# Kernel tuning notes

Hardware: AMD Instinct MI355X
Metric: run time of the kernel (lower is better)

## Reference

```python
import jax, jax.numpy as jnp
import numpy as np

N = 50000      # nodes
E = 800000     # edges (before self-loops)
H = 4          # attention heads
C = 32         # out_features per head
DIN = 128      # in_features (== H*C so residual path is active)
ED = 16        # edge_dim
NEG = 0.2      # LeakyReLU negative slope (GATConv default)
EPS = 1e-5     # LayerNorm eps


def setup_inputs() -> dict:
    key = jax.random.key(0)
    ks = jax.random.split(key, 12)
    s = 0.05
    return {
        "x": jax.random.normal(ks[0], (N, DIN), dtype=jnp.float32),
        "edge_index": jax.random.randint(ks[1], (2, E), 0, N, dtype=jnp.int64),
        "edge_attr": jax.random.normal(ks[2], (E, ED), dtype=jnp.float32),
        # edge_processor: Linear(ED, ED) + ReLU (dropout = identity at eval)
        "W_ep": jax.random.normal(ks[3], (ED, ED), dtype=jnp.float32) * s,
        "b_ep": jnp.zeros((ED,), dtype=jnp.float32),
        # GATConv params (lin / lin_edge are bias-free in PyG)
        "W_lin": jax.random.normal(ks[4], (DIN, H * C), dtype=jnp.float32) * s,
        "W_edge": jax.random.normal(ks[5], (ED, H * C), dtype=jnp.float32) * s,
        "att_src": jax.random.normal(ks[6], (H, C), dtype=jnp.float32) * s,
        "att_dst": jax.random.normal(ks[7], (H, C), dtype=jnp.float32) * s,
        "att_edge": jax.random.normal(ks[8], (H, C), dtype=jnp.float32) * s,
        "bias": jnp.zeros((H * C,), dtype=jnp.float32),
        # LayerNorm params
        "ln_g": jnp.ones((H * C,), dtype=jnp.float32),
        "ln_b": jnp.zeros((H * C,), dtype=jnp.float32),
    }


def reference(x, edge_index, edge_attr, W_ep, b_ep, W_lin, W_edge,
              att_src, att_dst, att_edge, bias, ln_g, ln_b):
    n = x.shape[0]
    src, dst = edge_index[0], edge_index[1]

    # edge_processor: Linear + ReLU
    ea = jax.nn.relu(edge_attr @ W_ep + b_ep)                       # [E, ED]

    # add self-loops (PyG GATConv default), loop edge_attr = mean of incoming
    ones = jnp.ones((ea.shape[0],), dtype=ea.dtype)
    deg = jax.ops.segment_sum(ones, dst, num_segments=n)            # [N]
    loop_attr = jax.ops.segment_sum(ea, dst, num_segments=n)
    loop_attr = loop_attr / jnp.maximum(deg, 1.0)[:, None]          # [N, ED]
    loop = jnp.arange(n, dtype=src.dtype)
    src2 = jnp.concatenate([src, loop])                             # [E+N]
    dst2 = jnp.concatenate([dst, loop])
    ea2 = jnp.concatenate([ea, loop_attr], axis=0)                  # [E+N, ED]

    # node / edge linear transforms
    h = (x @ W_lin).reshape(n, H, C)                                # [N, H, C]
    a_src = jnp.einsum('nhc,hc->nh', h, att_src)                    # [N, H]
    a_dst = jnp.einsum('nhc,hc->nh', h, att_dst)
    e = (ea2 @ W_edge).reshape(-1, H, C)                            # [E+N, H, C]
    a_e = jnp.einsum('ehc,hc->eh', e, att_edge)                     # [E+N, H]

    # per-edge attention logits + leaky relu
    alpha = a_src[src2] + a_dst[dst2] + a_e                         # [E+N, H]
    alpha = jnp.where(alpha >= 0, alpha, NEG * alpha)

    # segment softmax over incoming edges of each dst node
    m = jax.ops.segment_max(alpha, dst2, num_segments=n)            # [N, H]
    ex = jnp.exp(alpha - m[dst2])
    denom = jax.ops.segment_sum(ex, dst2, num_segments=n)           # [N, H]
    w = ex / denom[dst2]                                            # [E+N, H]

    # scatter-aggregate messages
    msg = h[src2] * w[:, :, None]                                   # [E+N, H, C]
    out = jax.ops.segment_sum(msg, dst2, num_segments=n)            # [N, H, C]
    out = out.reshape(n, H * C) + bias

    # residual (DIN == H*C) + LayerNorm
    out = out + x
    mu = jnp.mean(out, axis=-1, keepdims=True)
    var = jnp.var(out, axis=-1, keepdims=True)
    out = (out - mu) * jax.lax.rsqrt(var + EPS) * ln_g + ln_b
    return out
```

## Files before the change

kernel.cpp:

```cpp
#include <hip/hip_runtime.h>
#include <hip/hip_fp16.h>
#include <math.h>

#define NN   50000
#define EE   800000
#define HH   4
#define CC   32
#define DINN 128
#define ED   16
#define NEGS 0.2f
#define LNEPS 1e-5f
#define CPAD 32
#define SLOT 64

struct __align__(16) Hp4 { __half2 a, b, c, d; };

__global__ __launch_bounds__(256, 3) void k_node(
        const float* __restrict__ x, const float* __restrict__ W_lin,
        const float* __restrict__ att_src, const float* __restrict__ att_dst,
        __half* __restrict__ hb, float* __restrict__ a_src, float* __restrict__ a_dst,
        int* __restrict__ cnt) {
    __shared__ float xr[64 * 132];
    int t = threadIdx.x;
    int row0 = blockIdx.x * 64;

    #pragma unroll
    for (int i = 0; i < 8; ++i) {
        int idx = blockIdx.x * 2048 + i * 256 + t;
        if (idx < NN * CPAD) cnt[idx] = 0;
    }

    #pragma unroll
    for (int i = 0; i < 8; ++i) {
        int idx = t + 256 * i;
        int r = idx >> 5, kq = idx & 31;
        int row = row0 + r;
        float4 v = make_float4(0.f, 0.f, 0.f, 0.f);
        if (row < NN) v = ((const float4*)x)[(long)row * 32 + kq];
        *(float4*)&xr[r * 132 + kq * 4] = v;
    }
    __syncthreads();

    int colg = t & 15, rowg = t >> 4;
    int c0 = colg * 8;
    const float* Wp = W_lin + c0;
    float acc[4][8] = {};

    #pragma unroll 2
    for (int k = 0; k < DINN; k += 2) {
        float4 wa0 = *(const float4*)&Wp[(long)k * DINN];
        float4 wb0 = *(const float4*)&Wp[(long)k * DINN + 4];
        float4 wa1 = *(const float4*)&Wp[(long)(k + 1) * DINN];
        float4 wb1 = *(const float4*)&Wp[(long)(k + 1) * DINN + 4];
        #pragma unroll
        for (int i = 0; i < 4; ++i) {
            float2 xv = *(const float2*)&xr[(rowg * 4 + i) * 132 + k];
            acc[i][0] = fmaf(xv.x, wa0.x, acc[i][0]);
            acc[i][1] = fmaf(xv.x, wa0.y, acc[i][1]);
            acc[i][2] = fmaf(xv.x, wa0.z, acc[i][2]);
            acc[i][3] = fmaf(xv.x, wa0.w, acc[i][3]);
            acc[i][4] = fmaf(xv.x, wb0.x, acc[i][4]);
            acc[i][5] = fmaf(xv.x, wb0.y, acc[i][5]);
            acc[i][6] = fmaf(xv.x, wb0.z, acc[i][6]);
            acc[i][7] = fmaf(xv.x, wb0.w, acc[i][7]);
            acc[i][0] = fmaf(xv.y, wa1.x, acc[i][0]);
            acc[i][1] = fmaf(xv.y, wa1.y, acc[i][1]);
            acc[i][2] = fmaf(xv.y, wa1.z, acc[i][2]);
            acc[i][3] = fmaf(xv.y, wa1.w, acc[i][3]);
            acc[i][4] = fmaf(xv.y, wb1.x, acc[i][4]);
            acc[i][5] = fmaf(xv.y, wb1.y, acc[i][5]);
            acc[i][6] = fmaf(xv.y, wb1.z, acc[i][6]);
            acc[i][7] = fmaf(xv.y, wb1.w, acc[i][7]);
        }
    }

    int head = colg >> 2;
    int cw = c0 & 31;
    float4 as0 = *(const float4*)&att_src[head * CC + cw];
    float4 as1 = *(const float4*)&att_src[head * CC + cw + 4];
    float4 ad0 = *(const float4*)&att_dst[head * CC + cw];
    float4 ad1 = *(const float4*)&att_dst[head * CC + cw + 4];
    #pragma unroll
    for (int i = 0; i < 4; ++i) {
        int row = row0 + rowg * 4 + i;
        if (row < NN) {
            Hp4 p;
            p.a = __floats2half2_rn(acc[i][0], acc[i][1]);
            p.b = __floats2half2_rn(acc[i][2], acc[i][3]);
            p.c = __floats2half2_rn(acc[i][4], acc[i][5]);
            p.d = __floats2half2_rn(acc[i][6], acc[i][7]);
            *(Hp4*)&hb[(long)row * DINN + c0] = p;
        }
        float ps = acc[i][0]*as0.x + acc[i][1]*as0.y + acc[i][2]*as0.z + acc[i][3]*as0.w
                 + acc[i][4]*as1.x + acc[i][5]*as1.y + acc[i][6]*as1.z + acc[i][7]*as1.w;
        float pd = acc[i][0]*ad0.x + acc[i][1]*ad0.y + acc[i][2]*ad0.z + acc[i][3]*ad0.w
                 + acc[i][4]*ad1.x + acc[i][5]*ad1.y + acc[i][6]*ad1.z + acc[i][7]*ad1.w;
        ps += __shfl_xor(ps, 1); ps += __shfl_xor(ps, 2);
        pd += __shfl_xor(pd, 1); pd += __shfl_xor(pd, 2);
        if ((colg & 3) == 0 && row < NN) {
            a_src[row * 4 + head] = ps;
            a_dst[row * 4 + head] = pd;
        }
    }
}

__device__ __forceinline__ void edge_compute(
        float4 A0, float4 A1, float4 A2, float4 A3,
        const float* __restrict__ Wl, const float* __restrict__ bl,
        const float* __restrict__ vl,
        int src, int dst, int rk, uint4* __restrict__ pk) {
    float a[ED];
    a[0]=A0.x; a[1]=A0.y; a[2]=A0.z; a[3]=A0.w;
    a[4]=A1.x; a[5]=A1.y; a[6]=A1.z; a[7]=A1.w;
    a[8]=A2.x; a[9]=A2.y; a[10]=A2.z; a[11]=A2.w;
    a[12]=A3.x; a[13]=A3.y; a[14]=A3.z; a[15]=A3.w;

    float r[ED];
    #pragma unroll
    for (int j = 0; j < ED; ++j) r[j] = bl[j];
    #pragma unroll
    for (int d = 0; d < ED; ++d) {
        float av = a[d];
        #pragma unroll
        for (int j = 0; j < ED; ++j) r[j] = fmaf(av, Wl[d * ED + j], r[j]);
    }

    float ae0 = 0.f, ae1 = 0.f, ae2 = 0.f, ae3 = 0.f;
    #pragma unroll
    for (int d = 0; d < ED; ++d) {
        float rd = fmaxf(r[d], 0.f);
        ae0 = fmaf(rd, vl[d * 4 + 0], ae0);
        ae1 = fmaf(rd, vl[d * 4 + 1], ae1);
        ae2 = fmaf(rd, vl[d * 4 + 2], ae2);
        ae3 = fmaf(rd, vl[d * 4 + 3], ae3);
    }

    __half2 ae01 = __floats2half2_rn(ae0, ae1);
    __half2 ae23 = __floats2half2_rn(ae2, ae3);
    if (rk < SLOT) {
        long q = (long)dst * SLOT + rk;
        pk[q] = make_uint4(*(unsigned*)&ae01, *(unsigned*)&ae23,
                           (unsigned)src, 0u);
    }
}

__global__ __launch_bounds__(256) void k_edgeA(
        const int* __restrict__ ei, const float* __restrict__ edge_attr,
        const float* __restrict__ W_ep, const float* __restrict__ b_ep,
        const float* __restrict__ W_edge, const float* __restrict__ att_edge,
        int* __restrict__ cnt, uint4* __restrict__ pk) {
    __shared__ float Wl[ED * ED];
    __shared__ float bl[ED];
    __shared__ float vl[ED * 4];
    int t = threadIdx.x;
    if (t < ED * ED) Wl[t] = W_ep[t];
    if (t < ED) bl[t] = b_ep[t];
    if (t >= 192 && t < 192 + 64) {
        int q = t - 192;
        int d = q >> 2, h = q & 3;
        float s = 0.f;
        #pragma unroll 8
        for (int c = 0; c < CC; ++c)
            s += W_edge[d * (HH * CC) + h * CC + c] * att_edge[h * CC + c];
        vl[q] = s;
    }
    __syncthreads();

    int e0 = blockIdx.x * 512 + t;
    int e1 = e0 + 256;

    if ((blockIdx.x + 1) * 512 <= EE) {
        int s0 = ei[e0], s1 = ei[e1];
        int d0 = ei[EE + e0], d1 = ei[EE + e1];

        const float4* ap0 = (const float4*)(edge_attr + (long)e0 * ED);
        const float4* ap1 = (const float4*)(edge_attr + (long)e1 * ED);
        float4 A0 = ap0[0], A1 = ap0[1], A2 = ap0[2], A3 = ap0[3];
        float4 B0 = ap1[0], B1 = ap1[1], B2 = ap1[2], B3 = ap1[3];

        int rk0 = atomicAdd(cnt + (long)d0 * CPAD, 1);
        int rk1 = atomicAdd(cnt + (long)d1 * CPAD, 1);

        edge_compute(A0, A1, A2, A3, Wl, bl, vl, s0, d0, rk0, pk);
        edge_compute(B0, B1, B2, B3, Wl, bl, vl, s1, d1, rk1, pk);
    } else {
        #pragma unroll
        for (int u = 0; u < 2; ++u) {
            int e = e0 + u * 256;
            if (e >= EE) break;
            int src = ei[e];
            int dst = ei[EE + e];
            const float4* ap = (const float4*)(edge_attr + (long)e * ED);
            float4 A0 = ap[0], A1 = ap[1], A2 = ap[2], A3 = ap[3];
            int rk = atomicAdd(cnt + (long)dst * CPAD, 1);
            edge_compute(A0, A1, A2, A3, Wl, bl, vl, src, dst, rk, pk);
        }
    }
}

#define AGG_STEP(qq, hh, AA)                                      \
    do {                                                          \
        unsigned aw_ = (head & 2) ? (qq).y : (qq).x;              \
        float2 aef_ = __half22float2(*(__half2*)&aw_);            \
        float ae_ = (head & 1) ? aef_.y : aef_.x;                 \
        float v_ = (AA) + adn + ae_;                              \
        v_ = (v_ >= 0.f) ? v_ : NEGS * v_;                        \
        float w_ = __expf(v_);                                    \
        s_own += w_;                                              \
        aes_own += ae_;                                           \
        float2 hf_ = __half22float2(hh);                          \
        accx = fmaf(w_, hf_.x, accx);                             \
        accy = fmaf(w_, hf_.y, accy);                             \
    } while (0)

__global__ __launch_bounds__(256) void k_aggregate(
        const float* __restrict__ x, const __half2* __restrict__ hb,
        const float* __restrict__ a_src, const float* __restrict__ a_dst,
        const int* __restrict__ cnt, const uint4* __restrict__ pk,
        const float* __restrict__ bias, const float* __restrict__ ln_g,
        const float* __restrict__ ln_b, float* __restrict__ out) {
    int t = threadIdx.x;
    int wave = t >> 6, lane = t & 63;
    int n = blockIdx.x * 4 + wave;
    if (n >= NN) return;

    int deg = cnt[(long)n * CPAD];
    if (deg > SLOT) deg = SLOT;
    const uint4* rp = pk + (long)n * SLOT;
    int head = lane >> 4;

    float adn = a_dst[n * 4 + head];
    float accx = 0.f, accy = 0.f, s_own = 0.f, aes_own = 0.f;

    int k = 0;
    for (; k + 8 <= deg; k += 8) {
        uint4 q0 = rp[k + 0], q1 = rp[k + 1], q2 = rp[k + 2], q3 = rp[k + 3];
        uint4 q4 = rp[k + 4], q5 = rp[k + 5], q6 = rp[k + 6], q7 = rp[k + 7];
        int s0 = (int)q0.z, s1 = (int)q1.z, s2 = (int)q2.z, s3 = (int)q3.z;
        int s4 = (int)q4.z, s5 = (int)q5.z, s6 = (int)q6.z, s7 = (int)q7.z;
        __half2 h0 = hb[(long)s0 * 64 + lane], h1 = hb[(long)s1 * 64 + lane];
        __half2 h2 = hb[(long)s2 * 64 + lane], h3 = hb[(long)s3 * 64 + lane];
        __half2 h4 = hb[(long)s4 * 64 + lane], h5 = hb[(long)s5 * 64 + lane];
        __half2 h6 = hb[(long)s6 * 64 + lane], h7 = hb[(long)s7 * 64 + lane];
        float A0 = a_src[s0 * 4 + head], A1 = a_src[s1 * 4 + head];
        float A2 = a_src[s2 * 4 + head], A3 = a_src[s3 * 4 + head];
        float A4 = a_src[s4 * 4 + head], A5 = a_src[s5 * 4 + head];
        float A6 = a_src[s6 * 4 + head], A7 = a_src[s7 * 4 + head];
        AGG_STEP(q0, h0, A0); AGG_STEP(q1, h1, A1);
        AGG_STEP(q2, h2, A2); AGG_STEP(q3, h3, A3);
        AGG_STEP(q4, h4, A4); AGG_STEP(q5, h5, A5);
        AGG_STEP(q6, h6, A6); AGG_STEP(q7, h7, A7);
    }
    for (; k < deg; ++k) {
        uint4 q0 = rp[k];
        int s0 = (int)q0.z;
        __half2 h0 = hb[(long)s0 * 64 + lane];
        float A0 = a_src[s0 * 4 + head];
        AGG_STEP(q0, h0, A0);
    }

    float asn = a_src[n * 4 + head];
    float inv_deg = 1.0f / fmaxf((float)deg, 1.0f);
    float v = asn + adn + aes_own * inv_deg;
    v = (v >= 0.f) ? v : NEGS * v;
    float w0 = __expf(v);
    s_own += w0;
    float2 hn = __half22float2(hb[(long)n * 64 + lane]);
    accx = fmaf(w0, hn.x, accx);
    accy = fmaf(w0, hn.y, accy);
    float is = 1.0f / s_own;
    accx *= is; accy *= is;

    int c0 = lane * 2;
    float2 b2 = *(const float2*)&bias[c0];
    float2 x2 = *(const float2*)&x[(long)n * DINN + c0];
    float oa = accx + b2.x + x2.x;
    float ob = accy + b2.y + x2.y;
    float sum = oa + ob, sumsq = oa * oa + ob * ob;
    #pragma unroll
    for (int d2 = 1; d2 < 64; d2 <<= 1) {
        sum   += __shfl_xor(sum, d2);
        sumsq += __shfl_xor(sumsq, d2);
    }
    float mu  = sum * (1.0f / DINN);
    float var = sumsq * (1.0f / DINN) - mu * mu;
    float rs  = rsqrtf(var + LNEPS);
    float2 g2  = *(const float2*)&ln_g[c0];
    float2 lb2 = *(const float2*)&ln_b[c0];
    float2 o2;
    o2.x = (oa - mu) * rs * g2.x + lb2.x;
    o2.y = (ob - mu) * rs * g2.y + lb2.y;
    *(float2*)&out[(long)n * DINN + c0] = o2;
}

extern "C" void kernel_launch(void* const* d_in, const int* in_sizes, int n_in,
                              void* d_out, int out_size, void* d_ws, size_t ws_size,
                              hipStream_t stream) {
    const float* x         = (const float*)d_in[0];
    const int*   ei        = (const int*)d_in[1];
    const float* edge_attr = (const float*)d_in[2];
    const float* W_ep      = (const float*)d_in[3];
    const float* b_ep      = (const float*)d_in[4];
    const float* W_lin     = (const float*)d_in[5];
    const float* W_edge    = (const float*)d_in[6];
    const float* att_src   = (const float*)d_in[7];
    const float* att_dst   = (const float*)d_in[8];
    const float* att_edge  = (const float*)d_in[9];
    const float* bias      = (const float*)d_in[10];
    const float* ln_g      = (const float*)d_in[11];
    const float* ln_b      = (const float*)d_in[12];
    float* out = (float*)d_out;

    char* ws = (char*)d_ws;
    size_t o = 0;
    auto take = [&](size_t bytes) -> char* {
        char* p = ws + o;
        o = (o + bytes + 255) & ~(size_t)255;
        return p;
    };
    __half* hbuf  = (__half*)take((size_t)NN * DINN * 2);
    float*  a_src = (float*)take((size_t)NN * 4 * 4);
    float*  a_dst = (float*)take((size_t)NN * 4 * 4);
    int*    cnt   = (int*)  take((size_t)NN * CPAD * 4);
    uint4*  pk    = (uint4*)take((size_t)NN * SLOT * 16);

    k_node<<<(NN + 63) / 64, 256, 0, stream>>>(x, W_lin, att_src, att_dst,
                                               hbuf, a_src, a_dst, cnt);
    k_edgeA<<<(EE + 511) / 512, 256, 0, stream>>>(ei, edge_attr, W_ep, b_ep,
                                                  W_edge, att_edge, cnt, pk);
    k_aggregate<<<(NN + 3) / 4, 256, 0, stream>>>(x, (const __half2*)hbuf,
                                                  a_src, a_dst, cnt,
                                                  (const uint4*)pk,
                                                  bias, ln_g, ln_b, out);
}
```

Measured before the change: 268.9 us.

## Fuse node projection and edge kernels into one interleaved launch

Merges the node linear-projection kernel and the edge-processing kernel into a single launch. Every third block does node GEMM work and the rest do edge work, so the compute-heavy node blocks and the atomic/memory-heavy edge blocks can run concurrently and one kernel boundary disappears. Because edge blocks now increment counters while node blocks may still be running, counter zeroing moves to a separate hipMemsetAsync. In exchange, edge blocks now reserve the node path's large shared-memory buffer and share its launch bounds, which may lower their occupancy.

New measurement: 267.5 us. About the same (-0.5%).

```diff
diff --git a/kernel.cpp b/kernel.cpp
--- a/kernel.cpp
+++ b/kernel.cpp
@@ -13,96 +13,11 @@
 #define CPAD 32
 #define SLOT 64
 
+#define NBLK_NODE 782
+#define NBLK_EDGE 1563
+#define NBLK_FUSED (NBLK_NODE + NBLK_EDGE)
+
 struct __align__(16) Hp4 { __half2 a, b, c, d; };
-
-__global__ __launch_bounds__(256, 3) void k_node(
-        const float* __restrict__ x, const float* __restrict__ W_lin,
-        const float* __restrict__ att_src, const float* __restrict__ att_dst,
-        __half* __restrict__ hb, float* __restrict__ a_src, float* __restrict__ a_dst,
-        int* __restrict__ cnt) {
-    __shared__ float xr[64 * 132];
-    int t = threadIdx.x;
-    int row0 = blockIdx.x * 64;
-
-    #pragma unroll
-    for (int i = 0; i < 8; ++i) {
-        int idx = blockIdx.x * 2048 + i * 256 + t;
-        if (idx < NN * CPAD) cnt[idx] = 0;
-    }
-
-    #pragma unroll
-    for (int i = 0; i < 8; ++i) {
-        int idx = t + 256 * i;
-        int r = idx >> 5, kq = idx & 31;
-        int row = row0 + r;
-        float4 v = make_float4(0.f, 0.f, 0.f, 0.f);
-        if (row < NN) v = ((const float4*)x)[(long)row * 32 + kq];
-        *(float4*)&xr[r * 132 + kq * 4] = v;
-    }
-    __syncthreads();
-
-    int colg = t & 15, rowg = t >> 4;
-    int c0 = colg * 8;
-    const float* Wp = W_lin + c0;
-    float acc[4][8] = {};
-
-    #pragma unroll 2
-    for (int k = 0; k < DINN; k += 2) {
-        float4 wa0 = *(const float4*)&Wp[(long)k * DINN];
-        float4 wb0 = *(const float4*)&Wp[(long)k * DINN + 4];
-        float4 wa1 = *(const float4*)&Wp[(long)(k + 1) * DINN];
-        float4 wb1 = *(const float4*)&Wp[(long)(k + 1) * DINN + 4];
-        #pragma unroll
-        for (int i = 0; i < 4; ++i) {
-            float2 xv = *(const float2*)&xr[(rowg * 4 + i) * 132 + k];
-            acc[i][0] = fmaf(xv.x, wa0.x, acc[i][0]);
-            acc[i][1] = fmaf(xv.x, wa0.y, acc[i][1]);
-            acc[i][2] = fmaf(xv.x, wa0.z, acc[i][2]);
-            acc[i][3] = fmaf(xv.x, wa0.w, acc[i][3]);
-            acc[i][4] = fmaf(xv.x, wb0.x, acc[i][4]);
-            acc[i][5] = fmaf(xv.x, wb0.y, acc[i][5]);
-            acc[i][6] = fmaf(xv.x, wb0.z, acc[i][6]);
-            acc[i][7] = fmaf(xv.x, wb0.w, acc[i][7]);
-            acc[i][0] = fmaf(xv.y, wa1.x, acc[i][0]);
-            acc[i][1] = fmaf(xv.y, wa1.y, acc[i][1]);
-            acc[i][2] = fmaf(xv.y, wa1.z, acc[i][2]);
-            acc[i][3] = fmaf(xv.y, wa1.w, acc[i][3]);
-            acc[i][4] = fmaf(xv.y, wb1.x, acc[i][4]);
-            acc[i][5] = fmaf(xv.y, wb1.y, acc[i][5]);
-            acc[i][6] = fmaf(xv.y, wb1.z, acc[i][6]);
-            acc[i][7] = fmaf(xv.y, wb1.w, acc[i][7]);
-        }
-    }
-
-    int head = colg >> 2;
-    int cw = c0 & 31;
-    float4 as0 = *(const float4*)&att_src[head * CC + cw];
-    float4 as1 = *(const float4*)&att_src[head * CC + cw + 4];
-    float4 ad0 = *(const float4*)&att_dst[head * CC + cw];
-    float4 ad1 = *(const float4*)&att_dst[head * CC + cw + 4];
-    #pragma unroll
-    for (int i = 0; i < 4; ++i) {
-        int row = row0 + rowg * 4 + i;
-        if (row < NN) {
-            Hp4 p;
-            p.a = __floats2half2_rn(acc[i][0], acc[i][1]);
-            p.b = __floats2half2_rn(acc[i][2], acc[i][3]);
-            p.c = __floats2half2_rn(acc[i][4], acc[i][5]);
-            p.d = __floats2half2_rn(acc[i][6], acc[i][7]);
-            *(Hp4*)&hb[(long)row * DINN + c0] = p;
-        }
-        float ps = acc[i][0]*as0.x + acc[i][1]*as0.y + acc[i][2]*as0.z + acc[i][3]*as0.w
-                 + acc[i][4]*as1.x + acc[i][5]*as1.y + acc[i][6]*as1.z + acc[i][7]*as1.w;
-        float pd = acc[i][0]*ad0.x + acc[i][1]*ad0.y + acc[i][2]*ad0.z + acc[i][3]*ad0.w
-                 + acc[i][4]*ad1.x + acc[i][5]*ad1.y + acc[i][6]*ad1.z + acc[i][7]*ad1.w;
-        ps += __shfl_xor(ps, 1); ps += __shfl_xor(ps, 2);
-        pd += __shfl_xor(pd, 1); pd += __shfl_xor(pd, 2);
-        if ((colg & 3) == 0 && row < NN) {
-            a_src[row * 4 + head] = ps;
-            a_dst[row * 4 + head] = pd;
-        }
-    }
-}
 
 __device__ __forceinline__ void edge_compute(
         float4 A0, float4 A1, float4 A2, float4 A3,
@@ -144,56 +59,142 @@
     }
 }
 
-__global__ __launch_bounds__(256) void k_edgeA(
+__global__ __launch_bounds__(256, 3) void k_fused(
+        const float* __restrict__ x, const float* __restrict__ W_lin,
+        const float* __restrict__ att_src, const float* __restrict__ att_dst,
+        __half* __restrict__ hb, float* __restrict__ a_src, float* __restrict__ a_dst,
         const int* __restrict__ ei, const float* __restrict__ edge_attr,
         const float* __restrict__ W_ep, const float* __restrict__ b_ep,
         const float* __restrict__ W_edge, const float* __restrict__ att_edge,
         int* __restrict__ cnt, uint4* __restrict__ pk) {
-    __shared__ float Wl[ED * ED];
-    __shared__ float bl[ED];
-    __shared__ float vl[ED * 4];
+    __shared__ float smem[64 * 132];
+    int bid = blockIdx.x;
     int t = threadIdx.x;
-    if (t < ED * ED) Wl[t] = W_ep[t];
-    if (t < ED) bl[t] = b_ep[t];
-    if (t >= 192 && t < 192 + 64) {
-        int q = t - 192;
-        int d = q >> 2, h = q & 3;
-        float s = 0.f;
-        #pragma unroll 8
-        for (int c = 0; c < CC; ++c)
-            s += W_edge[d * (HH * CC) + h * CC + c] * att_edge[h * CC + c];
-        vl[q] = s;
-    }
-    __syncthreads();
-
-    int e0 = blockIdx.x * 512 + t;
-    int e1 = e0 + 256;
-
-    if ((blockIdx.x + 1) * 512 <= EE) {
-        int s0 = ei[e0], s1 = ei[e1];
-        int d0 = ei[EE + e0], d1 = ei[EE + e1];
-
-        const float4* ap0 = (const float4*)(edge_attr + (long)e0 * ED);
-        const float4* ap1 = (const float4*)(edge_attr + (long)e1 * ED);
-        float4 A0 = ap0[0], A1 = ap0[1], A2 = ap0[2], A3 = ap0[3];
-        float4 B0 = ap1[0], B1 = ap1[1], B2 = ap1[2], B3 = ap1[3];
-
-        int rk0 = atomicAdd(cnt + (long)d0 * CPAD, 1);
-        int rk1 = atomicAdd(cnt + (long)d1 * CPAD, 1);
-
-        edge_compute(A0, A1, A2, A3, Wl, bl, vl, s0, d0, rk0, pk);
-        edge_compute(B0, B1, B2, B3, Wl, bl, vl, s1, d1, rk1, pk);
+
+    if (bid % 3 == 0) {
+        float* xr = smem;
+        int row0 = (bid / 3) * 64;
+
+        #pragma unroll
+        for (int i = 0; i < 8; ++i) {
+            int idx = t + 256 * i;
+            int r = idx >> 5, kq = idx & 31;
+            int row = row0 + r;
+            float4 v = make_float4(0.f, 0.f, 0.f, 0.f);
+            if (row < NN) v = ((const float4*)x)[(long)row * 32 + kq];
+            *(float4*)&xr[r * 132 + kq * 4] = v;
+        }
+        __syncthreads();
+
+        int colg = t & 15, rowg = t >> 4;
+        int c0 = colg * 8;
+        const float* Wp = W_lin + c0;
+        float acc[4][8] = {};
+
+        #pragma unroll 2
+        for (int k = 0; k < DINN; k += 2) {
+            float4 wa0 = *(const float4*)&Wp[(long)k * DINN];
+            float4 wb0 = *(const float4*)&Wp[(long)k * DINN + 4];
+            float4 wa1 = *(const float4*)&Wp[(long)(k + 1) * DINN];
+            float4 wb1 = *(const float4*)&Wp[(long)(k + 1) * DINN + 4];
+            #pragma unroll
+            for (int i = 0; i < 4; ++i) {
+                float2 xv = *(const float2*)&xr[(rowg * 4 + i) * 132 + k];
+                acc[i][0] = fmaf(xv.x, wa0.x, acc[i][0]);
+                acc[i][1] = fmaf(xv.x, wa0.y, acc[i][1]);
+                acc[i][2] = fmaf(xv.x, wa0.z, acc[i][2]);
+                acc[i][3] = fmaf(xv.x, wa0.w, acc[i][3]);
+                acc[i][4] = fmaf(xv.x, wb0.x, acc[i][4]);
+                acc[i][5] = fmaf(xv.x, wb0.y, acc[i][5]);
+                acc[i][6] = fmaf(xv.x, wb0.z, acc[i][6]);
+                acc[i][7] = fmaf(xv.x, wb0.w, acc[i][7]);
+                acc[i][0] = fmaf(xv.y, wa1.x, acc[i][0]);
+                acc[i][1] = fmaf(xv.y, wa1.y, acc[i][1]);
+                acc[i][2] = fmaf(xv.y, wa1.z, acc[i][2]);
+                acc[i][3] = fmaf(xv.y, wa1.w, acc[i][3]);
+                acc[i][4] = fmaf(xv.y, wb1.x, acc[i][4]);
+                acc[i][5] = fmaf(xv.y, wb1.y, acc[i][5]);
+                acc[i][6] = fmaf(xv.y, wb1.z, acc[i][6]);
+                acc[i][7] = fmaf(xv.y, wb1.w, acc[i][7]);
+            }
+        }
+
+        int head = colg >> 2;
+        int cw = c0 & 31;
+        float4 as0 = *(const float4*)&att_src[head * CC + cw];
+        float4 as1 = *(const float4*)&att_src[head * CC + cw + 4];
+        float4 ad0 = *(const float4*)&att_dst[head * CC + cw];
+        float4 ad1 = *(const float4*)&att_dst[head * CC + cw + 4];
+        #pragma unroll
+        for (int i = 0; i < 4; ++i) {
+            int row = row0 + rowg * 4 + i;
+            if (row < NN) {
+                Hp4 p;
+                p.a = __floats2half2_rn(acc[i][0], acc[i][1]);
+                p.b = __floats2half2_rn(acc[i][2], acc[i][3]);
+                p.c = __floats2half2_rn(acc[i][4], acc[i][5]);
+                p.d = __floats2half2_rn(acc[i][6], acc[i][7]);
+                *(Hp4*)&hb[(long)row * DINN + c0] = p;
+            }
+            float ps = acc[i][0]*as0.x + acc[i][1]*as0.y + acc[i][2]*as0.z + acc[i][3]*as0.w
+                     + acc[i][4]*as1.x + acc[i][5]*as1.y + acc[i][6]*as1.z + acc[i][7]*as1.w;
+            float pd = acc[i][0]*ad0.x + acc[i][1]*ad0.y + acc[i][2]*ad0.z + acc[i][3]*ad0.w
+                     + acc[i][4]*ad1.x + acc[i][5]*ad1.y + acc[i][6]*ad1.z + acc[i][7]*ad1.w;
+            ps += __shfl_xor(ps, 1); ps += __shfl_xor(ps, 2);
+            pd += __shfl_xor(pd, 1); pd += __shfl_xor(pd, 2);
+            if ((colg & 3) == 0 && row < NN) {
+                a_src[row * 4 + head] = ps;
+                a_dst[row * 4 + head] = pd;
+            }
+        }
     } else {
-        #pragma unroll
-        for (int u = 0; u < 2; ++u) {
-            int e = e0 + u * 256;
-            if (e >= EE) break;
-            int src = ei[e];
-            int dst = ei[EE + e];
-            const float4* ap = (const float4*)(edge_attr + (long)e * ED);
-            float4 A0 = ap[0], A1 = ap[1], A2 = ap[2], A3 = ap[3];
-            int rk = atomicAdd(cnt + (long)dst * CPAD, 1);
-            edge_compute(A0, A1, A2, A3, Wl, bl, vl, src, dst, rk, pk);
+        float* Wl = smem;
+        float* bl = smem + 256;
+        float* vl = smem + 272;
+        int eb = bid - bid / 3 - 1;
+
+        if (t < ED * ED) Wl[t] = W_ep[t];
+        if (t < ED) bl[t] = b_ep[t];
+        if (t >= 192 && t < 192 + 64) {
+            int q = t - 192;
+            int d = q >> 2, h = q & 3;
+            float s = 0.f;
+            #pragma unroll 8
+            for (int c = 0; c < CC; ++c)
+                s += W_edge[d * (HH * CC) + h * CC + c] * att_edge[h * CC + c];
+            vl[q] = s;
+        }
+        __syncthreads();
+
+        int e0 = eb * 512 + t;
+        int e1 = e0 + 256;
+
+        if ((eb + 1) * 512 <= EE) {
+            int s0 = ei[e0], s1 = ei[e1];
+            int d0 = ei[EE + e0], d1 = ei[EE + e1];
+
+            const float4* ap0 = (const float4*)(edge_attr + (long)e0 * ED);
+            const float4* ap1 = (const float4*)(edge_attr + (long)e1 * ED);
+            float4 A0 = ap0[0], A1 = ap0[1], A2 = ap0[2], A3 = ap0[3];
+            float4 B0 = ap1[0], B1 = ap1[1], B2 = ap1[2], B3 = ap1[3];
+
+            int rk0 = atomicAdd(cnt + (long)d0 * CPAD, 1);
+            int rk1 = atomicAdd(cnt + (long)d1 * CPAD, 1);
+
+            edge_compute(A0, A1, A2, A3, Wl, bl, vl, s0, d0, rk0, pk);
+            edge_compute(B0, B1, B2, B3, Wl, bl, vl, s1, d1, rk1, pk);
+        } else {
+            #pragma unroll
+            for (int u = 0; u < 2; ++u) {
+                int e = e0 + u * 256;
+                if (e >= EE) break;
+                int src = ei[e];
+                int dst = ei[EE + e];
+                const float4* ap = (const float4*)(edge_attr + (long)e * ED);
+                float4 A0 = ap[0], A1 = ap[1], A2 = ap[2], A3 = ap[3];
+                int rk = atomicAdd(cnt + (long)dst * CPAD, 1);
+                edge_compute(A0, A1, A2, A3, Wl, bl, vl, src, dst, rk, pk);
+            }
         }
     }
 }
@@ -324,10 +325,12 @@
     int*    cnt   = (int*)  take((size_t)NN * CPAD * 4);
     uint4*  pk    = (uint4*)take((size_t)NN * SLOT * 16);
 
-    k_node<<<(NN + 63) / 64, 256, 0, stream>>>(x, W_lin, att_src, att_dst,
-                                               hbuf, a_src, a_dst, cnt);
-    k_edgeA<<<(EE + 511) / 512, 256, 0, stream>>>(ei, edge_attr, W_ep, b_ep,
-                                                  W_edge, att_edge, cnt, pk);
+    hipMemsetAsync(cnt, 0, (size_t)NN * CPAD * 4, stream);
+
+    k_fused<<<NBLK_FUSED, 256, 0, stream>>>(x, W_lin, att_src, att_dst,
+                                            hbuf, a_src, a_dst,
+                                            ei, edge_attr, W_ep, b_ep,
+                                            W_edge, att_edge, cnt, pk);
     k_aggregate<<<(NN + 3) / 4, 256, 0, stream>>>(x, (const __half2*)hbuf,
                                                   a_src, a_dst, cnt,
                                                   (const uint4*)pk,
```
